# Performance work log

Hardware: AMD Instinct MI355X
Metric: run time of the kernel (lower is better)

The kernel has to match this reference:

```python
import jax, jax.numpy as jnp
import numpy as np

NUM_ITERS = 3
EPS_ATTN = 1e-8
LN_EPS = 1e-3  # tf.keras LayerNormalization default epsilon


def layernorm(x, g, b):
    m = jnp.mean(x, axis=-1, keepdims=True)
    v = jnp.var(x, axis=-1, keepdims=True)
    return (x - m) * jax.lax.rsqrt(v + LN_EPS) * g + b


def setup_inputs() -> dict:
    key = jax.random.key(0)
    ks = jax.random.split(key, 20)
    B, N, Din, S, D, H = 64, 4096, 64, 7, 64, 128

    def glorot(k, shape):
        fan_in, fan_out = shape[-2], shape[-1]
        lim = np.sqrt(6.0 / (fan_in + fan_out))
        return jax.random.uniform(k, shape, jnp.float32, -lim, lim)

    return {
        "inputs": jax.random.normal(ks[0], (B, N, Din), jnp.float32),
        "slot_noise": jax.random.normal(ks[1], (B, S, D), jnp.float32),
        "ln_in_g": jnp.ones((Din,), jnp.float32), "ln_in_b": jnp.zeros((Din,), jnp.float32),
        "ln_s_g": jnp.ones((D,), jnp.float32), "ln_s_b": jnp.zeros((D,), jnp.float32),
        "ln_m_g": jnp.ones((D,), jnp.float32), "ln_m_b": jnp.zeros((D,), jnp.float32),
        "Wq": glorot(ks[2], (D, D)),
        "Wk": glorot(ks[3], (Din, D)),
        "Wv": glorot(ks[4], (Din, D)),
        "slots_mu": glorot(ks[5], (1, 1, D)),
        "slots_log_sigma": glorot(ks[6], (1, 1, D)),
        "gru_W": glorot(ks[7], (D, 3 * D)),
        "gru_U": glorot(ks[8], (D, 3 * D)),
        "gru_b": jnp.zeros((2, 3 * D), jnp.float32),  # [input_bias, recurrent_bias] (reset_after=True)
        "W1": glorot(ks[9], (D, H)), "b1": jnp.zeros((H,), jnp.float32),
        "W2": glorot(ks[10], (H, D)), "b2": jnp.zeros((D,), jnp.float32),
    }


def reference(inputs, slot_noise, ln_in_g, ln_in_b, ln_s_g, ln_s_b, ln_m_g, ln_m_b,
              Wq, Wk, Wv, slots_mu, slots_log_sigma, gru_W, gru_U, gru_b,
              W1, b1, W2, b2):
    D = Wq.shape[0]
    x = layernorm(inputs, ln_in_g, ln_in_b)          # [B,N,Din]
    k = x @ Wk                                       # [B,N,D]
    v = x @ Wv                                       # [B,N,D]
    slots = slots_mu + jnp.exp(slots_log_sigma) * slot_noise  # [B,S,D]

    scale = D ** (-0.5)
    for _ in range(NUM_ITERS):
        slots_prev = slots
        s = layernorm(slots, ln_s_g, ln_s_b)
        q = (s @ Wq) * scale                         # [B,S,D]
        logits = jnp.einsum("bnd,bsd->bns", k, q)   # [B,N,S]
        attn = jax.nn.softmax(logits, axis=-1) + EPS_ATTN
        attn = attn / jnp.sum(attn, axis=-2, keepdims=True)  # normalize over inputs N
        updates = jnp.einsum("bns,bnd->bsd", attn, v)        # [B,S,D]
        # GRUCell (Keras v2: reset_after=True, sigmoid recurrent activation)
        mx = updates @ gru_W + gru_b[0]
        mh = slots_prev @ gru_U + gru_b[1]
        xz, xr, xh = jnp.split(mx, 3, axis=-1)
        hz, hr, hh = jnp.split(mh, 3, axis=-1)
        z = jax.nn.sigmoid(xz + hz)
        r = jax.nn.sigmoid(xr + hr)
        hcand = jnp.tanh(xh + r * hh)
        slots = z * slots_prev + (1.0 - z) * hcand
        # MLP with residual
        m = layernorm(slots, ln_m_g, ln_m_b)
        slots = slots + jax.nn.relu(m @ W1 + b1) @ W2 + b2
    return slots
```

## Files before the change

### kernel.cpp

```cpp
#include <hip/hip_runtime.h>
#include <hip/hip_bf16.h>


#define NB 64
#define NN 4096
#define NS 7
#define LN_EPS 1e-3f
#define EPS_ATTN 1e-8f

typedef __attribute__((ext_vector_type(8))) __bf16 bf16x8;
typedef __attribute__((ext_vector_type(8))) unsigned short u16x8;
typedef __attribute__((ext_vector_type(4))) float f32x4;
typedef __attribute__((ext_vector_type(4))) unsigned int u32x4;

__device__ __forceinline__ unsigned short f2bf(float f) {
    unsigned int x = __float_as_uint(f);
    x += 0x7FFFu + ((x >> 16) & 1u);
    return (unsigned short)(x >> 16);
}

__device__ __forceinline__ bf16x8 pack8(float4 a, float4 b) {
    u16x8 r;
    r[0] = f2bf(a.x); r[1] = f2bf(a.y); r[2] = f2bf(a.z); r[3] = f2bf(a.w);
    r[4] = f2bf(b.x); r[5] = f2bf(b.y); r[6] = f2bf(b.z); r[7] = f2bf(b.w);
    return __builtin_bit_cast(bf16x8, r);
}

__global__ __launch_bounds__(64) void prep_kernel(
        const float* __restrict__ Wk, const float* __restrict__ Wv,
        const float* __restrict__ g, const float* __restrict__ bb,
        unsigned short* __restrict__ GkT, unsigned short* __restrict__ GvT,
        float* __restrict__ cgk, float* __restrict__ cbk,
        float* __restrict__ cgv, float* __restrict__ cbv) {
    int j = blockIdx.x & 63, mat = blockIdx.x >> 6, d = threadIdx.x;
    const float* W = mat ? Wv : Wk;
    unsigned short* GT = mat ? GvT : GkT;
    float* cg = mat ? cgv : cgk;
    float* cb = mat ? cbv : cbk;
    float w = W[d * 64 + j];
    float gv = g[d], bv = bb[d];
    GT[j * 64 + d] = f2bf(gv * w);
    float sg = gv * w, sb = bv * w;
#pragma unroll
    for (int off = 1; off < 64; off <<= 1) {
        sg += __shfl_xor(sg, off);
        sb += __shfl_xor(sb, off);
    }
    if (d == 0) { cg[j] = sg; cb[j] = sb; }
}

__global__ void init_slots_kernel(const float* __restrict__ noise, const float* __restrict__ mu,
                                  const float* __restrict__ lsig, float* __restrict__ slots) {
    int idx = blockIdx.x * 256 + threadIdx.x;
    if (idx < NB * NS * 64) {
        int d = idx & 63;
        slots[idx] = mu[d] + __expf(lsig[d]) * noise[idx];
    }
}

__global__ __launch_bounds__(256) void proj_kernel(
        const float* __restrict__ x, const unsigned short* __restrict__ GkT,
        const unsigned short* __restrict__ GvT,
        const float* __restrict__ cgk, const float* __restrict__ cbk,
        const float* __restrict__ cgv, const float* __restrict__ cbv,
        unsigned short* __restrict__ kout, unsigned short* __restrict__ vT) {
    int t = threadIdx.x;
    int w = t >> 6, lane = t & 63;
    int h = lane >> 4, rl = lane & 15;
    long base = (long)blockIdx.x * 128;
    int bb = blockIdx.x >> 5;
    int nblk = (blockIdx.x & 31) * 128;
    const float* xr0 = x + (base + w * 16 + rl) * 64 + h * 8;
    const float* xr1 = xr0 + 64 * 64;
    float4 xa[8];
    xa[0] = *(const float4*)(xr0);      xa[1] = *(const float4*)(xr0 + 4);
    xa[2] = *(const float4*)(xr0 + 32); xa[3] = *(const float4*)(xr0 + 36);
    xa[4] = *(const float4*)(xr1);      xa[5] = *(const float4*)(xr1 + 4);
    xa[6] = *(const float4*)(xr1 + 32); xa[7] = *(const float4*)(xr1 + 36);
    float s1a = 0.f, s2a = 0.f, s1b = 0.f, s2b = 0.f;
#pragma unroll
    for (int i = 0; i < 4; ++i) {
        s1a += xa[i].x + xa[i].y + xa[i].z + xa[i].w;
        s2a += xa[i].x * xa[i].x + xa[i].y * xa[i].y + xa[i].z * xa[i].z + xa[i].w * xa[i].w;
        s1b += xa[4 + i].x + xa[4 + i].y + xa[4 + i].z + xa[4 + i].w;
        s2b += xa[4 + i].x * xa[4 + i].x + xa[4 + i].y * xa[4 + i].y + xa[4 + i].z * xa[4 + i].z + xa[4 + i].w * xa[4 + i].w;
    }
    s1a += __shfl_xor(s1a, 16); s2a += __shfl_xor(s2a, 16);
    s1a += __shfl_xor(s1a, 32); s2a += __shfl_xor(s2a, 32);
    s1b += __shfl_xor(s1b, 16); s2b += __shfl_xor(s2b, 16);
    s1b += __shfl_xor(s1b, 32); s2b += __shfl_xor(s2b, 32);
    float m0 = s1a * (1.f / 64.f);
    float i0 = rsqrtf(s2a * (1.f / 64.f) - m0 * m0 + LN_EPS);
    float m1 = s1b * (1.f / 64.f);
    float i1 = rsqrtf(s2b * (1.f / 64.f) - m1 * m1 + LN_EPS);
    bf16x8 a00 = pack8(xa[0], xa[1]), a01 = pack8(xa[2], xa[3]);
    bf16x8 a10 = pack8(xa[4], xa[5]), a11 = pack8(xa[6], xa[7]);
    f32x4 k0a[4], v0a[4], k1a[4], v1a[4];
#pragma unroll
    for (int nt = 0; nt < 4; ++nt) {
        k0a[nt] = (f32x4){0.f, 0.f, 0.f, 0.f}; v0a[nt] = (f32x4){0.f, 0.f, 0.f, 0.f};
        k1a[nt] = (f32x4){0.f, 0.f, 0.f, 0.f}; v1a[nt] = (f32x4){0.f, 0.f, 0.f, 0.f};
    }
#pragma unroll
    for (int nt = 0; nt < 4; ++nt) {
        const unsigned short* gk = GkT + (nt * 16 + rl) * 64 + h * 8;
        const unsigned short* gv = GvT + (nt * 16 + rl) * 64 + h * 8;
        bf16x8 bk0 = *(const bf16x8*)(gk);
        bf16x8 bk1 = *(const bf16x8*)(gk + 32);
        bf16x8 bv0 = *(const bf16x8*)(gv);
        bf16x8 bv1 = *(const bf16x8*)(gv + 32);
        k0a[nt] = __builtin_amdgcn_mfma_f32_16x16x32_bf16(a00, bk0, k0a[nt], 0, 0, 0);
        k0a[nt] = __builtin_amdgcn_mfma_f32_16x16x32_bf16(a01, bk1, k0a[nt], 0, 0, 0);
        v0a[nt] = __builtin_amdgcn_mfma_f32_16x16x32_bf16(a00, bv0, v0a[nt], 0, 0, 0);
        v0a[nt] = __builtin_amdgcn_mfma_f32_16x16x32_bf16(a01, bv1, v0a[nt], 0, 0, 0);
        k1a[nt] = __builtin_amdgcn_mfma_f32_16x16x32_bf16(a10, bk0, k1a[nt], 0, 0, 0);
        k1a[nt] = __builtin_amdgcn_mfma_f32_16x16x32_bf16(a11, bk1, k1a[nt], 0, 0, 0);
        v1a[nt] = __builtin_amdgcn_mfma_f32_16x16x32_bf16(a10, bv0, v1a[nt], 0, 0, 0);
        v1a[nt] = __builtin_amdgcn_mfma_f32_16x16x32_bf16(a11, bv1, v1a[nt], 0, 0, 0);
    }
    float mr0[4], ir0[4], mr1[4], ir1[4];
#pragma unroll
    for (int r = 0; r < 4; ++r) {
        int rlsrc = h * 4 + r;
        mr0[r] = __shfl(m0, rlsrc); ir0[r] = __shfl(i0, rlsrc);
        mr1[r] = __shfl(m1, rlsrc); ir1[r] = __shfl(i1, rlsrc);
    }
#pragma unroll
    for (int nt = 0; nt < 4; ++nt) {
        int j = nt * 16 + rl;
        float cgkj = cgk[j], cbkj = cbk[j], cgvj = cgv[j], cbvj = cbv[j];
        unsigned int vp0 = 0, vp1 = 0;
#pragma unroll
        for (int r = 0; r < 4; ++r) {
            long row = base + w * 16 + h * 4 + r;
            kout[row * 64 + j] = f2bf(ir0[r] * (k0a[nt][r] - mr0[r] * cgkj) + cbkj);
            unsigned int vb = f2bf(ir0[r] * (v0a[nt][r] - mr0[r] * cgvj) + cbvj);
            if (r < 2) vp0 |= vb << (16 * r); else vp1 |= vb << (16 * (r - 2));
        }
        {
            long vaddr = ((long)(bb * 64 + j)) * NN + nblk + w * 16 + h * 4;
            *(uint2*)(vT + vaddr) = make_uint2(vp0, vp1);
        }
        vp0 = 0; vp1 = 0;
#pragma unroll
        for (int r = 0; r < 4; ++r) {
            long row = base + 64 + w * 16 + h * 4 + r;
            kout[row * 64 + j] = f2bf(ir1[r] * (k1a[nt][r] - mr1[r] * cgkj) + cbkj);
            unsigned int vb = f2bf(ir1[r] * (v1a[nt][r] - mr1[r] * cgvj) + cbvj);
            if (r < 2) vp0 |= vb << (16 * r); else vp1 |= vb << (16 * (r - 2));
        }
        {
            long vaddr = ((long)(bb * 64 + j)) * NN + nblk + 64 + w * 16 + h * 4;
            *(uint2*)(vT + vaddr) = make_uint2(vp0, vp1);
        }
    }
}

__global__ __launch_bounds__(64) void slots_pre_kernel(
        const float* __restrict__ slots, const float* __restrict__ Wq,
        const float* __restrict__ lg, const float* __restrict__ lb,
        float* __restrict__ q, float* __restrict__ U, float* __restrict__ Z) {
    __shared__ float sn[64];
    int bs = blockIdx.x, d = threadIdx.x;
    float xv = slots[bs * 64 + d];
    float s1 = xv, s2 = xv * xv;
#pragma unroll
    for (int off = 1; off < 64; off <<= 1) {
        s1 += __shfl_xor(s1, off);
        s2 += __shfl_xor(s2, off);
    }
    float m = s1 * (1.f / 64.f);
    float inv = rsqrtf(s2 * (1.f / 64.f) - m * m + LN_EPS);
    sn[d] = (xv - m) * inv * lg[d] + lb[d];
    __syncthreads();
    float acc = 0.f;
#pragma unroll 8
    for (int i = 0; i < 64; ++i) acc += sn[i] * Wq[i * 64 + d];
    q[bs * 64 + d] = acc * 0.125f;
    U[bs * 64 + d] = 0.f;
    if (d == 0) Z[bs] = 0.f;
}

__global__ __launch_bounds__(256) void attn_kernel(
        const unsigned short* __restrict__ kp, const unsigned short* __restrict__ vtp,
        const float* __restrict__ q, float* __restrict__ U, float* __restrict__ Z) {
    __shared__ unsigned int plds[4][320];
    __shared__ float ured[4][512];
    int t = threadIdx.x;
    int b = blockIdx.x >> 4, blk = blockIdx.x & 15;
    int w = t >> 6, lane = t & 63;
    int h = lane >> 4, c = lane & 15;
    bf16x8 qf0, qf1;
    {
        int cs = (c < 7) ? c : 0;
        const float* qr = q + (b * NS + cs) * 64 + h * 8;
        float4 q0 = *(const float4*)(qr);
        float4 q1 = *(const float4*)(qr + 4);
        float4 q2 = *(const float4*)(qr + 32);
        float4 q3 = *(const float4*)(qr + 36);
        if (c >= 7) {
            q0 = make_float4(0.f, 0.f, 0.f, 0.f); q1 = q0; q2 = q0; q3 = q0;
        }
        qf0 = pack8(q0, q1);
        qf1 = pack8(q2, q3);
    }
    f32x4 pv[4];
#pragma unroll
    for (int i = 0; i < 4; ++i) pv[i] = (f32x4){0.f, 0.f, 0.f, 0.f};
    float zac = 0.f;
    unsigned int* pw = plds[w];
    long rb0 = (long)b * NN + blk * 256 + w * 16;
#pragma unroll
    for (int p = 0; p < 2; ++p) {
#pragma unroll
        for (int sh = 0; sh < 2; ++sh) {
            long rowbase = rb0 + p * 128 + sh * 64;
            const unsigned short* ka = kp + (rowbase + c) * 64 + h * 8;
            bf16x8 a0 = *(const bf16x8*)(ka);
            bf16x8 a1 = *(const bf16x8*)(ka + 32);
            f32x4 lg = (f32x4){0.f, 0.f, 0.f, 0.f};
            lg = __builtin_amdgcn_mfma_f32_16x16x32_bf16(a0, qf0, lg, 0, 0, 0);
            lg = __builtin_amdgcn_mfma_f32_16x16x32_bf16(a1, qf1, lg, 0, 0, 0);
            float av[4];
#pragma unroll
            for (int j = 0; j < 4; ++j) {
                float vl = (c < 7) ? lg[j] : -1e30f;
                float mx = vl;
                mx = fmaxf(mx, __shfl_xor(mx, 1));
                mx = fmaxf(mx, __shfl_xor(mx, 2));
                mx = fmaxf(mx, __shfl_xor(mx, 4));
                mx = fmaxf(mx, __shfl_xor(mx, 8));
                float e = (c < 7) ? __expf(lg[j] - mx) : 0.f;
                float se = e;
                se += __shfl_xor(se, 1);
                se += __shfl_xor(se, 2);
                se += __shfl_xor(se, 4);
                se += __shfl_xor(se, 8);
                float a = (c < 7) ? (__fdividef(e, se) + EPS_ATTN) : 0.f;
                av[j] = a;
                zac += a;
            }
            unsigned int w0 = (unsigned int)f2bf(av[0]) | ((unsigned int)f2bf(av[1]) << 16);
            unsigned int w1 = (unsigned int)f2bf(av[2]) | ((unsigned int)f2bf(av[3]) << 16);
            pw[c * 20 + sh * 8 + 2 * h]     = w0;
            pw[c * 20 + sh * 8 + 2 * h + 1] = w1;
        }
        u32x4 pr = *(u32x4*)(&pw[c * 20 + 4 * h]);
        bf16x8 pa = __builtin_bit_cast(bf16x8, pr);
        int nb = blk * 256 + p * 128 + ((h < 2) ? (w * 16 + 8 * h) : (48 + w * 16 + 8 * h));
#pragma unroll
        for (int tile = 0; tile < 4; ++tile) {
            const unsigned short* vb = vtp + ((long)(b * 64 + tile * 16 + c)) * NN + nb;
            bf16x8 bv = *(const bf16x8*)(vb);
            pv[tile] = __builtin_amdgcn_mfma_f32_16x16x32_bf16(pa, bv, pv[tile], 0, 0, 0);
        }
    }
    zac += __shfl_xor(zac, 16);
    zac += __shfl_xor(zac, 32);
    if (h == 0 && c < 7) atomicAdd(Z + b * NS + c, zac);
    if (h < 2) {
#pragma unroll
        for (int tile = 0; tile < 4; ++tile) {
#pragma unroll
            for (int j = 0; j < 4; ++j) {
                ured[w][(4 * h + j) * 64 + tile * 16 + c] = pv[tile][j];
            }
        }
    }
    __syncthreads();
    for (int idx = t; idx < NS * 64; idx += 256) {
        float tot = ured[0][idx] + ured[1][idx] + ured[2][idx] + ured[3][idx];
        atomicAdd(U + b * NS * 64 + idx, tot);
    }
}

__global__ __launch_bounds__(256) void slots_post_kernel(
        float* __restrict__ slots, float* __restrict__ U, float* __restrict__ Z,
        const float* __restrict__ gW, const float* __restrict__ gU, const float* __restrict__ gb,
        const float* __restrict__ lmg, const float* __restrict__ lmb,
        const float* __restrict__ W1, const float* __restrict__ b1,
        const float* __restrict__ W2, const float* __restrict__ b2,
        const float* __restrict__ Wq, const float* __restrict__ lsg, const float* __restrict__ lsb,
        float* __restrict__ q, float* __restrict__ outp, int last) {
    __shared__ float up[64], hp[64], mx[192], mh[192], mm[64], hl[128], sn[64];
    int bs = blockIdx.x, t = threadIdx.x;
    if (t < 64) {
        float zsum = Z[bs];
        up[t] = U[bs * 64 + t] / zsum;
        hp[t] = slots[bs * 64 + t];
        U[bs * 64 + t] = 0.f;
        if (t == 0) Z[bs] = 0.f;
    }
    __syncthreads();
    if (t < 192) {
        float xa0 = gb[t], ha0 = gb[192 + t], xa1 = 0.f, ha1 = 0.f;
#pragma unroll 8
        for (int i = 0; i < 64; i += 2) {
            xa0 += up[i] * gW[i * 192 + t];
            ha0 += hp[i] * gU[i * 192 + t];
            xa1 += up[i + 1] * gW[(i + 1) * 192 + t];
            ha1 += hp[i + 1] * gU[(i + 1) * 192 + t];
        }
        mx[t] = xa0 + xa1; mh[t] = ha0 + ha1;
    }
    __syncthreads();
    float hnew = 0.f;
    if (t < 64) {
        float z = 1.f / (1.f + __expf(-(mx[t] + mh[t])));
        float r = 1.f / (1.f + __expf(-(mx[64 + t] + mh[64 + t])));
        float pre = mx[128 + t] + r * mh[128 + t];
        pre = fminf(fmaxf(pre, -15.f), 15.f);
        float e2 = __expf(2.f * pre);
        float hc = (e2 - 1.f) / (e2 + 1.f);
        hnew = z * hp[t] + (1.f - z) * hc;
        float s1 = hnew, s2 = hnew * hnew;
#pragma unroll
        for (int off = 1; off < 64; off <<= 1) { s1 += __shfl_xor(s1, off); s2 += __shfl_xor(s2, off); }
        float m = s1 * (1.f / 64.f);
        float inv = rsqrtf(s2 * (1.f / 64.f) - m * m + LN_EPS);
        mm[t] = (hnew - m) * inv * lmg[t] + lmb[t];
    }
    __syncthreads();
    if (t < 128) {
        float h1 = b1[t], h2 = 0.f;
#pragma unroll 8
        for (int i = 0; i < 64; i += 2) {
            h1 += mm[i] * W1[i * 128 + t];
            h2 += mm[i + 1] * W1[(i + 1) * 128 + t];
        }
        hl[t] = fmaxf(h1 + h2, 0.f);
    }
    __syncthreads();
    if (t < 64) {
        float o = hnew + b2[t], o1 = 0.f;
#pragma unroll 8
        for (int j = 0; j < 128; j += 2) {
            o += hl[j] * W2[j * 64 + t];
            o1 += hl[j + 1] * W2[(j + 1) * 64 + t];
        }
        o += o1;
        slots[bs * 64 + t] = o;
        if (last) outp[bs * 64 + t] = o;
        float s1 = o, s2 = o * o;
#pragma unroll
        for (int off = 1; off < 64; off <<= 1) { s1 += __shfl_xor(s1, off); s2 += __shfl_xor(s2, off); }
        float m = s1 * (1.f / 64.f);
        float inv = rsqrtf(s2 * (1.f / 64.f) - m * m + LN_EPS);
        sn[t] = (o - m) * inv * lsg[t] + lsb[t];
    }
    __syncthreads();
    if (t < 64) {
        float acc = 0.f;
#pragma unroll 8
        for (int i = 0; i < 64; ++i) acc += sn[i] * Wq[i * 64 + t];
        q[bs * 64 + t] = acc * 0.125f;
    }
}

extern "C" void kernel_launch(void* const* d_in, const int* in_sizes, int n_in,
                              void* d_out, int out_size, void* d_ws, size_t ws_size,
                              hipStream_t stream) {
    const float* inputs  = (const float*)d_in[0];
    const float* noise   = (const float*)d_in[1];
    const float* ln_in_g = (const float*)d_in[2];
    const float* ln_in_b = (const float*)d_in[3];
    const float* ln_s_g  = (const float*)d_in[4];
    const float* ln_s_b  = (const float*)d_in[5];
    const float* ln_m_g  = (const float*)d_in[6];
    const float* ln_m_b  = (const float*)d_in[7];
    const float* Wq      = (const float*)d_in[8];
    const float* Wk      = (const float*)d_in[9];
    const float* Wv      = (const float*)d_in[10];
    const float* mu      = (const float*)d_in[11];
    const float* lsig    = (const float*)d_in[12];
    const float* gW      = (const float*)d_in[13];
    const float* gU      = (const float*)d_in[14];
    const float* gb      = (const float*)d_in[15];
    const float* W1      = (const float*)d_in[16];
    const float* b1      = (const float*)d_in[17];
    const float* W2      = (const float*)d_in[18];
    const float* b2      = (const float*)d_in[19];

    char* ws = (char*)d_ws;
    unsigned short* kbuf = (unsigned short*)ws;
    unsigned short* vtbuf = (unsigned short*)(ws + 33554432);
    float* slots = (float*)(ws + 67108864);
    float* qbuf  = (float*)(ws + 67108864 + 114688);
    float* Ubuf  = (float*)(ws + 67108864 + 2 * 114688);
    float* Zbuf  = (float*)(ws + 67108864 + 3 * 114688);
    unsigned short* GkT = (unsigned short*)(ws + 67108864 + 3 * 114688 + 4096);
    unsigned short* GvT = GkT + 4096;
    float* cgk = (float*)(GvT + 4096);
    float* cbk = cgk + 64;
    float* cgv = cbk + 64;
    float* cbv = cgv + 64;

    prep_kernel<<<128, 64, 0, stream>>>(Wk, Wv, ln_in_g, ln_in_b, GkT, GvT, cgk, cbk, cgv, cbv);
    init_slots_kernel<<<112, 256, 0, stream>>>(noise, mu, lsig, slots);
    proj_kernel<<<2048, 256, 0, stream>>>(inputs, GkT, GvT, cgk, cbk, cgv, cbv, kbuf, vtbuf);
    slots_pre_kernel<<<448, 64, 0, stream>>>(slots, Wq, ln_s_g, ln_s_b, qbuf, Ubuf, Zbuf);
    for (int it = 0; it < 3; ++it) {
        attn_kernel<<<1024, 256, 0, stream>>>(kbuf, vtbuf, qbuf, Ubuf, Zbuf);
        slots_post_kernel<<<448, 256, 0, stream>>>(slots, Ubuf, Zbuf, gW, gU, gb,
                                                   ln_m_g, ln_m_b, W1, b1, W2, b2,
                                                   Wq, ln_s_g, ln_s_b, qbuf,
                                                   (float*)d_out, (it == 2) ? 1 : 0);
    }
}
```

Baseline: 256.5 us.

## Stage projection outputs and V tiles through LDS, batch slot update per batch

```diff
diff --git a/kernel.cpp b/kernel.cpp
--- a/kernel.cpp
+++ b/kernel.cpp
@@ -64,6 +64,8 @@
         const float* __restrict__ cgk, const float* __restrict__ cbk,
         const float* __restrict__ cgv, const float* __restrict__ cbv,
         unsigned short* __restrict__ kout, unsigned short* __restrict__ vT) {
+    __shared__ __align__(16) unsigned short ktile[128 * 72];
+    __shared__ __align__(16) unsigned short vtile[64 * 136];
     int t = threadIdx.x;
     int w = t >> 6, lane = t & 63;
     int h = lane >> 4, rl = lane & 15;
@@ -129,30 +131,32 @@
     for (int nt = 0; nt < 4; ++nt) {
         int j = nt * 16 + rl;
         float cgkj = cgk[j], cbkj = cbk[j], cgvj = cgv[j], cbvj = cbv[j];
-        unsigned int vp0 = 0, vp1 = 0;
+        unsigned short vv0[4], vv1[4];
 #pragma unroll
         for (int r = 0; r < 4; ++r) {
-            long row = base + w * 16 + h * 4 + r;
-            kout[row * 64 + j] = f2bf(ir0[r] * (k0a[nt][r] - mr0[r] * cgkj) + cbkj);
-            unsigned int vb = f2bf(ir0[r] * (v0a[nt][r] - mr0[r] * cgvj) + cbvj);
-            if (r < 2) vp0 |= vb << (16 * r); else vp1 |= vb << (16 * (r - 2));
-        }
-        {
-            long vaddr = ((long)(bb * 64 + j)) * NN + nblk + w * 16 + h * 4;
-            *(uint2*)(vT + vaddr) = make_uint2(vp0, vp1);
-        }
-        vp0 = 0; vp1 = 0;
-#pragma unroll
-        for (int r = 0; r < 4; ++r) {
-            long row = base + 64 + w * 16 + h * 4 + r;
-            kout[row * 64 + j] = f2bf(ir1[r] * (k1a[nt][r] - mr1[r] * cgkj) + cbkj);
-            unsigned int vb = f2bf(ir1[r] * (v1a[nt][r] - mr1[r] * cgvj) + cbvj);
-            if (r < 2) vp0 |= vb << (16 * r); else vp1 |= vb << (16 * (r - 2));
-        }
-        {
-            long vaddr = ((long)(bb * 64 + j)) * NN + nblk + 64 + w * 16 + h * 4;
-            *(uint2*)(vT + vaddr) = make_uint2(vp0, vp1);
-        }
+            int row = w * 16 + h * 4 + r;
+            ktile[row * 72 + j] = f2bf(ir0[r] * (k0a[nt][r] - mr0[r] * cgkj) + cbkj);
+            ktile[(64 + row) * 72 + j] = f2bf(ir1[r] * (k1a[nt][r] - mr1[r] * cgkj) + cbkj);
+            vv0[r] = f2bf(ir0[r] * (v0a[nt][r] - mr0[r] * cgvj) + cbvj);
+            vv1[r] = f2bf(ir1[r] * (v1a[nt][r] - mr1[r] * cgvj) + cbvj);
+        }
+        uint2 p0 = make_uint2((unsigned int)vv0[0] | ((unsigned int)vv0[1] << 16),
+                              (unsigned int)vv0[2] | ((unsigned int)vv0[3] << 16));
+        uint2 p1 = make_uint2((unsigned int)vv1[0] | ((unsigned int)vv1[1] << 16),
+                              (unsigned int)vv1[2] | ((unsigned int)vv1[3] << 16));
+        *(uint2*)(&vtile[j * 136 + w * 16 + h * 4]) = p0;
+        *(uint2*)(&vtile[j * 136 + 64 + w * 16 + h * 4]) = p1;
+    }
+    __syncthreads();
+#pragma unroll
+    for (int i = 0; i < 4; ++i) {
+        int flat = (i * 256 + t) * 8;
+        int row = flat >> 6, col = flat & 63;
+        uint4 kd = *(const uint4*)(&ktile[row * 72 + col]);
+        *(uint4*)(kout + (base + row) * 64 + col) = kd;
+        int dd = flat >> 7, noff = flat & 127;
+        uint4 vd = *(const uint4*)(&vtile[dd * 136 + noff]);
+        *(uint4*)(vT + ((long)(bb * 64 + dd)) * NN + nblk + noff) = vd;
     }
 }
 
@@ -184,12 +188,20 @@
 __global__ __launch_bounds__(256) void attn_kernel(
         const unsigned short* __restrict__ kp, const unsigned short* __restrict__ vtp,
         const float* __restrict__ q, float* __restrict__ U, float* __restrict__ Z) {
-    __shared__ unsigned int plds[4][320];
-    __shared__ float ured[4][512];
+    __shared__ __align__(16) char smemraw[38912];
+    unsigned short* vtile = (unsigned short*)smemraw;
+    unsigned int* plds = (unsigned int*)(smemraw + 33792);
     int t = threadIdx.x;
     int b = blockIdx.x >> 4, blk = blockIdx.x & 15;
     int w = t >> 6, lane = t & 63;
     int h = lane >> 4, c = lane & 15;
+#pragma unroll
+    for (int i = 0; i < 8; ++i) {
+        int flat = (i * 256 + t) * 8;
+        int dd = flat >> 8, noff = flat & 255;
+        uint4 vv = *(const uint4*)(vtp + ((long)(b * 64 + dd)) * NN + blk * 256 + noff);
+        *(uint4*)(&vtile[dd * 264 + noff]) = vv;
+    }
     bf16x8 qf0, qf1;
     {
         int cs = (c < 7) ? c : 0;
@@ -208,8 +220,9 @@
 #pragma unroll
     for (int i = 0; i < 4; ++i) pv[i] = (f32x4){0.f, 0.f, 0.f, 0.f};
     float zac = 0.f;
-    unsigned int* pw = plds[w];
+    unsigned int* pw = plds + w * 320;
     long rb0 = (long)b * NN + blk * 256 + w * 16;
+    __syncthreads();
 #pragma unroll
     for (int p = 0; p < 2; ++p) {
 #pragma unroll
@@ -247,34 +260,35 @@
         }
         u32x4 pr = *(u32x4*)(&pw[c * 20 + 4 * h]);
         bf16x8 pa = __builtin_bit_cast(bf16x8, pr);
-        int nb = blk * 256 + p * 128 + ((h < 2) ? (w * 16 + 8 * h) : (48 + w * 16 + 8 * h));
+        int nloc = p * 128 + ((h < 2) ? (w * 16 + 8 * h) : (48 + w * 16 + 8 * h));
 #pragma unroll
         for (int tile = 0; tile < 4; ++tile) {
-            const unsigned short* vb = vtp + ((long)(b * 64 + tile * 16 + c)) * NN + nb;
-            bf16x8 bv = *(const bf16x8*)(vb);
+            bf16x8 bv = *(const bf16x8*)(&vtile[(tile * 16 + c) * 264 + nloc]);
             pv[tile] = __builtin_amdgcn_mfma_f32_16x16x32_bf16(pa, bv, pv[tile], 0, 0, 0);
         }
     }
     zac += __shfl_xor(zac, 16);
     zac += __shfl_xor(zac, 32);
     if (h == 0 && c < 7) atomicAdd(Z + b * NS + c, zac);
+    __syncthreads();
+    float* ured = (float*)smemraw;
     if (h < 2) {
 #pragma unroll
         for (int tile = 0; tile < 4; ++tile) {
 #pragma unroll
             for (int j = 0; j < 4; ++j) {
-                ured[w][(4 * h + j) * 64 + tile * 16 + c] = pv[tile][j];
+                ured[w * 512 + (4 * h + j) * 64 + tile * 16 + c] = pv[tile][j];
             }
         }
     }
     __syncthreads();
     for (int idx = t; idx < NS * 64; idx += 256) {
-        float tot = ured[0][idx] + ured[1][idx] + ured[2][idx] + ured[3][idx];
+        float tot = ured[idx] + ured[512 + idx] + ured[1024 + idx] + ured[1536 + idx];
         atomicAdd(U + b * NS * 64 + idx, tot);
     }
 }
 
-__global__ __launch_bounds__(256) void slots_post_kernel(
+__global__ __launch_bounds__(512) void slots_post_kernel(
         float* __restrict__ slots, float* __restrict__ U, float* __restrict__ Z,
         const float* __restrict__ gW, const float* __restrict__ gU, const float* __restrict__ gb,
         const float* __restrict__ lmg, const float* __restrict__ lmb,
@@ -282,78 +296,113 @@
         const float* __restrict__ W2, const float* __restrict__ b2,
         const float* __restrict__ Wq, const float* __restrict__ lsg, const float* __restrict__ lsb,
         float* __restrict__ q, float* __restrict__ outp, int last) {
-    __shared__ float up[64], hp[64], mx[192], mh[192], mm[64], hl[128], sn[64];
-    int bs = blockIdx.x, t = threadIdx.x;
-    if (t < 64) {
+    __shared__ float up[7][64], hp[7][64], hn[7][64], mm[7][64], sl[7][64], sn[7][64];
+    __shared__ float hl[7][128];
+    __shared__ float mxs[7][192], mhs[7][192];
+    int bq = blockIdx.x;
+    int t = threadIdx.x;
+    int s = t >> 6, d = t & 63;
+    if (t < 448) {
+        int bs = bq * 7 + s;
         float zsum = Z[bs];
-        up[t] = U[bs * 64 + t] / zsum;
-        hp[t] = slots[bs * 64 + t];
-        U[bs * 64 + t] = 0.f;
-        if (t == 0) Z[bs] = 0.f;
+        up[s][d] = U[bs * 64 + d] / zsum;
+        hp[s][d] = slots[bs * 64 + d];
+        U[bs * 64 + d] = 0.f;
+        if (d == 0) Z[bs] = 0.f;
     }
     __syncthreads();
     if (t < 192) {
-        float xa0 = gb[t], ha0 = gb[192 + t], xa1 = 0.f, ha1 = 0.f;
-#pragma unroll 8
-        for (int i = 0; i < 64; i += 2) {
-            xa0 += up[i] * gW[i * 192 + t];
-            ha0 += hp[i] * gU[i * 192 + t];
-            xa1 += up[i + 1] * gW[(i + 1) * 192 + t];
-            ha1 += hp[i + 1] * gU[(i + 1) * 192 + t];
-        }
-        mx[t] = xa0 + xa1; mh[t] = ha0 + ha1;
-    }
-    __syncthreads();
-    float hnew = 0.f;
-    if (t < 64) {
-        float z = 1.f / (1.f + __expf(-(mx[t] + mh[t])));
-        float r = 1.f / (1.f + __expf(-(mx[64 + t] + mh[64 + t])));
-        float pre = mx[128 + t] + r * mh[128 + t];
+        float acc[7];
+#pragma unroll
+        for (int s2 = 0; s2 < 7; ++s2) acc[s2] = gb[t];
+#pragma unroll 4
+        for (int i = 0; i < 64; ++i) {
+            float wv = gW[i * 192 + t];
+#pragma unroll
+            for (int s2 = 0; s2 < 7; ++s2) acc[s2] += up[s2][i] * wv;
+        }
+#pragma unroll
+        for (int s2 = 0; s2 < 7; ++s2) mxs[s2][t] = acc[s2];
+    } else if (t >= 256 && t < 448) {
+        int cc = t - 256;
+        float acc[7];
+#pragma unroll
+        for (int s2 = 0; s2 < 7; ++s2) acc[s2] = gb[192 + cc];
+#pragma unroll 4
+        for (int i = 0; i < 64; ++i) {
+            float wv = gU[i * 192 + cc];
+#pragma unroll
+            for (int s2 = 0; s2 < 7; ++s2) acc[s2] += hp[s2][i] * wv;
+        }
+#pragma unroll
+        for (int s2 = 0; s2 < 7; ++s2) mhs[s2][cc] = acc[s2];
+    }
+    __syncthreads();
+    if (t < 448) {
+        float z = 1.f / (1.f + __expf(-(mxs[s][d] + mhs[s][d])));
+        float r = 1.f / (1.f + __expf(-(mxs[s][64 + d] + mhs[s][64 + d])));
+        float pre = mxs[s][128 + d] + r * mhs[s][128 + d];
         pre = fminf(fmaxf(pre, -15.f), 15.f);
         float e2 = __expf(2.f * pre);
         float hc = (e2 - 1.f) / (e2 + 1.f);
-        hnew = z * hp[t] + (1.f - z) * hc;
-        float s1 = hnew, s2 = hnew * hnew;
-#pragma unroll
-        for (int off = 1; off < 64; off <<= 1) { s1 += __shfl_xor(s1, off); s2 += __shfl_xor(s2, off); }
+        float hnew = z * hp[s][d] + (1.f - z) * hc;
+        hn[s][d] = hnew;
+        float s1 = hnew, s2v = hnew * hnew;
+#pragma unroll
+        for (int off = 1; off < 64; off <<= 1) { s1 += __shfl_xor(s1, off); s2v += __shfl_xor(s2v, off); }
         float m = s1 * (1.f / 64.f);
-        float inv = rsqrtf(s2 * (1.f / 64.f) - m * m + LN_EPS);
-        mm[t] = (hnew - m) * inv * lmg[t] + lmb[t];
+        float inv = rsqrtf(s2v * (1.f / 64.f) - m * m + LN_EPS);
+        mm[s][d] = (hnew - m) * inv * lmg[d] + lmb[d];
     }
     __syncthreads();
     if (t < 128) {
-        float h1 = b1[t], h2 = 0.f;
-#pragma unroll 8
-        for (int i = 0; i < 64; i += 2) {
-            h1 += mm[i] * W1[i * 128 + t];
-            h2 += mm[i + 1] * W1[(i + 1) * 128 + t];
-        }
-        hl[t] = fmaxf(h1 + h2, 0.f);
+        float acc[7];
+#pragma unroll
+        for (int s2 = 0; s2 < 7; ++s2) acc[s2] = b1[t];
+#pragma unroll 4
+        for (int i = 0; i < 64; ++i) {
+            float wv = W1[i * 128 + t];
+#pragma unroll
+            for (int s2 = 0; s2 < 7; ++s2) acc[s2] += mm[s2][i] * wv;
+        }
+#pragma unroll
+        for (int s2 = 0; s2 < 7; ++s2) hl[s2][t] = fmaxf(acc[s2], 0.f);
     }
     __syncthreads();
     if (t < 64) {
-        float o = hnew + b2[t], o1 = 0.f;
-#pragma unroll 8
-        for (int j = 0; j < 128; j += 2) {
-            o += hl[j] * W2[j * 64 + t];
-            o1 += hl[j + 1] * W2[(j + 1) * 64 + t];
-        }
-        o += o1;
-        slots[bs * 64 + t] = o;
-        if (last) outp[bs * 64 + t] = o;
-        float s1 = o, s2 = o * o;
-#pragma unroll
-        for (int off = 1; off < 64; off <<= 1) { s1 += __shfl_xor(s1, off); s2 += __shfl_xor(s2, off); }
+        float acc[7];
+#pragma unroll
+        for (int s2 = 0; s2 < 7; ++s2) acc[s2] = hn[s2][t] + b2[t];
+#pragma unroll 4
+        for (int j = 0; j < 128; ++j) {
+            float wv = W2[j * 64 + t];
+#pragma unroll
+            for (int s2 = 0; s2 < 7; ++s2) acc[s2] += hl[s2][j] * wv;
+        }
+#pragma unroll
+        for (int s2 = 0; s2 < 7; ++s2) {
+            int bs = bq * 7 + s2;
+            slots[bs * 64 + t] = acc[s2];
+            if (last) outp[bs * 64 + t] = acc[s2];
+            sl[s2][t] = acc[s2];
+        }
+    }
+    __syncthreads();
+    if (t < 448) {
+        float o = sl[s][d];
+        float s1 = o, s2v = o * o;
+#pragma unroll
+        for (int off = 1; off < 64; off <<= 1) { s1 += __shfl_xor(s1, off); s2v += __shfl_xor(s2v, off); }
         float m = s1 * (1.f / 64.f);
-        float inv = rsqrtf(s2 * (1.f / 64.f) - m * m + LN_EPS);
-        sn[t] = (o - m) * inv * lsg[t] + lsb[t];
-    }
-    __syncthreads();
-    if (t < 64) {
+        float inv = rsqrtf(s2v * (1.f / 64.f) - m * m + LN_EPS);
+        sn[s][d] = (o - m) * inv * lsg[d] + lsb[d];
+    }
+    __syncthreads();
+    if (t < 448) {
         float acc = 0.f;
 #pragma unroll 8
-        for (int i = 0; i < 64; ++i) acc += sn[i] * Wq[i * 64 + t];
-        q[bs * 64 + t] = acc * 0.125f;
+        for (int i = 0; i < 64; ++i) acc += sn[s][i] * Wq[i * 64 + d];
+        q[(bq * 7 + s) * 64 + d] = acc * 0.125f;
     }
 }
 
@@ -401,9 +450,9 @@
     slots_pre_kernel<<<448, 64, 0, stream>>>(slots, Wq, ln_s_g, ln_s_b, qbuf, Ubuf, Zbuf);
     for (int it = 0; it < 3; ++it) {
         attn_kernel<<<1024, 256, 0, stream>>>(kbuf, vtbuf, qbuf, Ubuf, Zbuf);
-        slots_post_kernel<<<448, 256, 0, stream>>>(slots, Ubuf, Zbuf, gW, gU, gb,
-                                                   ln_m_g, ln_m_b, W1, b1, W2, b2,
-                                                   Wq, ln_s_g, ln_s_b, qbuf,
-                                                   (float*)d_out, (it == 2) ? 1 : 0);
-    }
-}
+        slots_post_kernel<<<64, 512, 0, stream>>>(slots, Ubuf, Zbuf, gW, gU, gb,
+                                                  ln_m_g, ln_m_b, W1, b1, W2, b2,
+                                                  Wq, ln_s_g, ln_s_b, qbuf,
+                                                  (float*)d_out, (it == 2) ? 1 : 0);
+    }
+}
```

New measurement: 302.2 us. 17.8% more time.
